# Kernel optimization log

Hardware: AMD Instinct MI355X
Metric: run time of the kernel (lower is better)

## Reference

```python
import jax, jax.numpy as jnp
import numpy as np

N = 200000       # num nodes
D = 128          # embedding dim
E_POS = 262144   # positive edges
NUM_NEGS = 4
E_NEG = E_POS * NUM_NEGS


def setup_inputs() -> dict:
    key = jax.random.key(0)
    k1, k2, k3, k4, k5 = jax.random.split(key, 5)
    h = jax.random.normal(k1, (N, D), dtype=jnp.float32)
    pos_src = jax.random.randint(k2, (E_POS,), 0, N, dtype=jnp.int32)
    pos_dst = jax.random.randint(k3, (E_POS,), 0, N, dtype=jnp.int32)
    neg_src = jax.random.randint(k4, (E_NEG,), 0, N, dtype=jnp.int32)
    neg_dst = jax.random.randint(k5, (E_NEG,), 0, N, dtype=jnp.int32)
    return {"h": h, "pos_src": pos_src, "pos_dst": pos_dst,
            "neg_src": neg_src, "neg_dst": neg_dst, "num_negs": NUM_NEGS}


def _edge_dot(h, src, dst):
    # SDDMM: gather src/dst rows, per-edge dot product -> [E]
    return jnp.einsum('ed,ed->e', h[src], h[dst])


def reference(h, pos_src, pos_dst, neg_src, neg_dst, num_negs):
    pos_score = _edge_dot(h, pos_src, pos_dst)   # [E_pos]
    neg_score = _edge_dot(h, neg_src, neg_dst)   # [E_neg]

    # BCE with logits: labels 1 for pos, 0 for neg
    score = jnp.concatenate([pos_score, neg_score])
    label = jnp.concatenate([jnp.ones_like(pos_score), jnp.zeros_like(neg_score)])
    loss = jnp.mean(jax.nn.softplus(score) - label * score)

    # MRR: rank of the positive among [pos | negs]
    mat = jnp.concatenate([pos_score[:, None],
                           neg_score.reshape(-1, num_negs)], axis=-1)  # [E_pos, 1+num_negs]
    order = jnp.argsort(-mat, axis=-1)          # indices_of_ranks (descending)
    ranks = jnp.argsort(order, axis=-1)[:, 0] + 1  # rank position of the positive
    mrr = jnp.mean(1.0 / ranks.astype(jnp.float32))
    return loss, mrr
```

## Files before the change

kernel.cpp:

```cpp
#include <hip/hip_runtime.h>
#include <math.h>

constexpr int NBLK    = 2048;
constexpr int CVT_BLK = 4096;

typedef float floatx2 __attribute__((ext_vector_type(2)));

#if __has_builtin(__builtin_amdgcn_cvt_pk_f32_fp8) && __has_builtin(__builtin_amdgcn_cvt_pk_fp8_f32)
#define HAVE_FP8_CVT 1
#else
#define HAVE_FP8_CVT 0
#endif

__device__ __forceinline__ float softplus_fast(float x) {
    float t = __expf(-fabsf(x));
    return fmaxf(x, 0.0f) + __logf(1.0f + t);
}


#if HAVE_FP8_CVT
__device__ __forceinline__ unsigned pack4_fp8(float x, float y, float z, float w) {
    int r = 0;
    r = __builtin_amdgcn_cvt_pk_fp8_f32(x, y, r, false);
    r = __builtin_amdgcn_cvt_pk_fp8_f32(z, w, r, true);
    return (unsigned)r;
}
__device__ __forceinline__ float dot_word_fp8(unsigned wa, unsigned wb, float c) {
    floatx2 a0 = __builtin_amdgcn_cvt_pk_f32_fp8((int)wa, false);
    floatx2 a1 = __builtin_amdgcn_cvt_pk_f32_fp8((int)wa, true);
    floatx2 b0 = __builtin_amdgcn_cvt_pk_f32_fp8((int)wb, false);
    floatx2 b1 = __builtin_amdgcn_cvt_pk_f32_fp8((int)wb, true);
    c = fmaf(a0.x, b0.x, c); c = fmaf(a0.y, b0.y, c);
    c = fmaf(a1.x, b1.x, c); c = fmaf(a1.y, b1.y, c);
    return c;
}
#else
__device__ __forceinline__ unsigned enc1_fp8(float f) {
    unsigned u = __float_as_uint(f);
    unsigned s = (u >> 24) & 0x80u;
    float a = fabsf(f);
    if (a < 0.001953125f) return s;
    if (a > 448.0f) a = 448.0f;
    unsigned b = __float_as_uint(a);
    unsigned exp = b >> 23;
    unsigned m = b & 0x7fffffu;
    unsigned mr = m >> 20, rest = m & 0xfffffu;
    if (rest > 0x80000u || (rest == 0x80000u && (mr & 1u))) mr++;
    if (mr == 8u) { mr = 0u; exp++; }
    int e8 = (int)exp - 127 + 7;
    if (e8 <= 0) return s;
    if (e8 > 15) { e8 = 15; mr = 6u; }
    return s | ((unsigned)e8 << 3) | mr;
}
__device__ __forceinline__ unsigned pack4_fp8(float x, float y, float z, float w) {
    return enc1_fp8(x) | (enc1_fp8(y) << 8) | (enc1_fp8(z) << 16) | (enc1_fp8(w) << 24);
}
__device__ __forceinline__ float dec1_fp8(unsigned v) {
    unsigned s = (v & 0x80u) << 24;
    unsigned em = v & 0x7fu;
    float mag;
    if (em < 8u) mag = (float)em * 0.001953125f;
    else         mag = __uint_as_float((em << 20) + (120u << 23));
    return __uint_as_float(s | __float_as_uint(mag));
}
__device__ __forceinline__ float dot_word_fp8(unsigned wa, unsigned wb, float c) {
    #pragma unroll
    for (int k = 0; k < 4; ++k)
        c = fmaf(dec1_fp8((wa >> (8 * k)) & 0xffu),
                 dec1_fp8((wb >> (8 * k)) & 0xffu), c);
    return c;
}
#endif

__device__ __forceinline__ float dot8_fp8_rows(const unsigned char* __restrict__ h8,
                                               int si, int di, int sub) {
    const uint2* ra = (const uint2*)(h8 + ((size_t)(unsigned)si << 7));
    const uint2* rb = (const uint2*)(h8 + ((size_t)(unsigned)di << 7));
    uint2 a = ra[sub];
    uint2 b = rb[sub];
    float c = dot_word_fp8(a.x, b.x, 0.0f);
    return  dot_word_fp8(a.y, b.y, c);
}

__global__ __launch_bounds__(256) void fused_kernel_8(
        const unsigned char* __restrict__ h8,
        const int* __restrict__ pos_src, const int* __restrict__ pos_dst,
        const int* __restrict__ neg_src, const int* __restrict__ neg_dst,
        float* __restrict__ out, int e_pos, float inv_total, float inv_epos) {
    const int lane = threadIdx.x & 63;
    const int warp = threadIdx.x >> 6;
    const int grp  = lane >> 4;
    const int sub  = lane & 15;
    const int gid0    = (blockIdx.x * (blockDim.x >> 6) + warp) * 4 + grp;
    const int gstride = gridDim.x * (blockDim.x >> 6) * 4;

    float loss_acc = 0.0f, mrr_acc = 0.0f;

    for (int i = gid0; i < e_pos; i += gstride) {
        int  ps = pos_src[i], pd = pos_dst[i];
        int4 ns = ((const int4*)neg_src)[i];
        int4 nd = ((const int4*)neg_dst)[i];

        float c0 = dot8_fp8_rows(h8, ps,   pd,   sub);
        float c1 = dot8_fp8_rows(h8, ns.x, nd.x, sub);
        float c2 = dot8_fp8_rows(h8, ns.y, nd.y, sub);
        float c3 = dot8_fp8_rows(h8, ns.z, nd.z, sub);
        float c4 = dot8_fp8_rows(h8, ns.w, nd.w, sub);

        #pragma unroll
        for (int off = 1; off <= 8; off <<= 1) {
            c0 += __shfl_xor(c0, off, 64);
            c1 += __shfl_xor(c1, off, 64);
            c2 += __shfl_xor(c2, off, 64);
            c3 += __shfl_xor(c3, off, 64);
            c4 += __shfl_xor(c4, off, 64);
        }
        if (sub == 0) {
            loss_acc += softplus_fast(-c0) + softplus_fast(c1) + softplus_fast(c2)
                      + softplus_fast(c3) + softplus_fast(c4);
            int r = 1 + (c1 > c0) + (c2 > c0) + (c3 > c0) + (c4 > c0);
            mrr_acc += 1.0f / (float)r;
        }
    }

    #pragma unroll
    for (int off = 1; off <= 32; off <<= 1) {
        loss_acc += __shfl_xor(loss_acc, off, 64);
        mrr_acc  += __shfl_xor(mrr_acc,  off, 64);
    }
    __shared__ float sl[4], sm[4];
    if (lane == 0) { sl[warp] = loss_acc; sm[warp] = mrr_acc; }
    __syncthreads();
    if (threadIdx.x == 0) {
        atomicAdd(&out[0], (sl[0] + sl[1] + sl[2] + sl[3]) * inv_total);
        atomicAdd(&out[1], (sm[0] + sm[1] + sm[2] + sm[3]) * inv_epos);
    }
}


__device__ __forceinline__ float dot_row_f(const float* __restrict__ h,
                                           int si, int di, int sub) {
    const float4* ra = (const float4*)((const char*)h + ((size_t)(unsigned)si << 9));
    const float4* rb = (const float4*)((const char*)h + ((size_t)(unsigned)di << 9));
    float4 a0 = ra[2*sub], a1 = ra[2*sub+1];
    float4 b0 = rb[2*sub], b1 = rb[2*sub+1];
    float c = a0.x*b0.x;
    c = fmaf(a0.y,b0.y,c); c = fmaf(a0.z,b0.z,c); c = fmaf(a0.w,b0.w,c);
    c = fmaf(a1.x,b1.x,c); c = fmaf(a1.y,b1.y,c);
    c = fmaf(a1.z,b1.z,c); c = fmaf(a1.w,b1.w,c);
    return c;
}

__global__ __launch_bounds__(256) void fused_kernel_f(
        const float* __restrict__ h,
        const int* __restrict__ pos_src, const int* __restrict__ pos_dst,
        const int* __restrict__ neg_src, const int* __restrict__ neg_dst,
        float* __restrict__ out, int e_pos, float inv_total, float inv_epos) {
    const int lane = threadIdx.x & 63;
    const int warp = threadIdx.x >> 6;
    const int grp  = lane >> 4;
    const int sub  = lane & 15;
    const int gid0    = (blockIdx.x * (blockDim.x >> 6) + warp) * 4 + grp;
    const int gstride = gridDim.x * (blockDim.x >> 6) * 4;

    float loss_acc = 0.0f, mrr_acc = 0.0f;
    for (int i = gid0; i < e_pos; i += gstride) {
        int  ps = pos_src[i], pd = pos_dst[i];
        int4 ns = ((const int4*)neg_src)[i];
        int4 nd = ((const int4*)neg_dst)[i];
        float c0 = dot_row_f(h, ps,   pd,   sub);
        float c1 = dot_row_f(h, ns.x, nd.x, sub);
        float c2 = dot_row_f(h, ns.y, nd.y, sub);
        float c3 = dot_row_f(h, ns.z, nd.z, sub);
        float c4 = dot_row_f(h, ns.w, nd.w, sub);
        #pragma unroll
        for (int off = 1; off <= 8; off <<= 1) {
            c0 += __shfl_xor(c0, off, 64);
            c1 += __shfl_xor(c1, off, 64);
            c2 += __shfl_xor(c2, off, 64);
            c3 += __shfl_xor(c3, off, 64);
            c4 += __shfl_xor(c4, off, 64);
        }
        if (sub == 0) {
            loss_acc += softplus_fast(-c0) + softplus_fast(c1) + softplus_fast(c2)
                      + softplus_fast(c3) + softplus_fast(c4);
            int r = 1 + (c1 > c0) + (c2 > c0) + (c3 > c0) + (c4 > c0);
            mrr_acc += 1.0f / (float)r;
        }
    }
    #pragma unroll
    for (int off = 1; off <= 32; off <<= 1) {
        loss_acc += __shfl_xor(loss_acc, off, 64);
        mrr_acc  += __shfl_xor(mrr_acc,  off, 64);
    }
    __shared__ float sl[4], sm[4];
    if (lane == 0) { sl[warp] = loss_acc; sm[warp] = mrr_acc; }
    __syncthreads();
    if (threadIdx.x == 0) {
        atomicAdd(&out[0], (sl[0] + sl[1] + sl[2] + sl[3]) * inv_total);
        atomicAdd(&out[1], (sm[0] + sm[1] + sm[2] + sm[3]) * inv_epos);
    }
}


__global__ __launch_bounds__(256) void convert_kernel_8(
        const float* __restrict__ h, unsigned char* __restrict__ h8, int n,
        float* __restrict__ out) {
    if (blockIdx.x == 0 && threadIdx.x == 0) { out[0] = 0.0f; out[1] = 0.0f; }
    const int tid    = blockIdx.x * blockDim.x + threadIdx.x;
    const int stride = gridDim.x * blockDim.x;
    const float4* h4 = (const float4*)h;
    uint2* o2 = (uint2*)h8;
    const int n8 = n >> 3;
    for (int i = tid; i < n8; i += stride) {
        float4 v0 = h4[2 * i];
        float4 v1 = h4[2 * i + 1];
        uint2 o;
        o.x = pack4_fp8(v0.x, v0.y, v0.z, v0.w);
        o.y = pack4_fp8(v1.x, v1.y, v1.z, v1.w);
        o2[i] = o;
    }
}

__global__ void zero_out_kernel(float* __restrict__ out) {
    out[0] = 0.0f; out[1] = 0.0f;
}

extern "C" void kernel_launch(void* const* d_in, const int* in_sizes, int n_in,
                              void* d_out, int out_size, void* d_ws, size_t ws_size,
                              hipStream_t stream) {
    const float* h       = (const float*)d_in[0];
    const int*   pos_src = (const int*)d_in[1];
    const int*   pos_dst = (const int*)d_in[2];
    const int*   neg_src = (const int*)d_in[3];
    const int*   neg_dst = (const int*)d_in[4];
    const int n_h   = in_sizes[0];
    const int e_pos = in_sizes[1];
    const int e_neg = in_sizes[3];
    float* out = (float*)d_out;

    const float inv_total = 1.0f / (float)((long long)e_pos + e_neg);
    const float inv_epos  = 1.0f / (float)e_pos;

    if (ws_size >= (size_t)n_h) {
        unsigned char* h8 = (unsigned char*)d_ws;
        convert_kernel_8<<<CVT_BLK, 256, 0, stream>>>(h, h8, n_h, out);
        fused_kernel_8<<<NBLK, 256, 0, stream>>>(
            h8, pos_src, pos_dst, neg_src, neg_dst,
            out, e_pos, inv_total, inv_epos);
    } else {
        zero_out_kernel<<<1, 1, 0, stream>>>(out);
        fused_kernel_f<<<NBLK, 256, 0, stream>>>(
            h, pos_src, pos_dst, neg_src, neg_dst,
            out, e_pos, inv_total, inv_epos);
    }
}
```

Before: 239.1 us.

## Use 8 lanes per edge with 16-byte row loads and prefetch next indices

Each edge group shrinks from 16 to 8 lanes, and each lane loads a uint4 (16 fp8 values) per row instead of a uint2. This widens the gather loads and halves the shuffle-reduction depth. The next iteration's edge indices are now loaded one iteration ahead (software pipelining) to hide index-load latency before the dependent row gathers. In exchange, each lane does twice the fp8 decode work and uses more registers, which may reduce occupancy.

Result: no change. 236.5 us (-1.1%).

```diff
diff --git a/kernel.cpp b/kernel.cpp
--- a/kernel.cpp
+++ b/kernel.cpp
@@ -72,14 +72,11 @@
 }
 #endif
 
-__device__ __forceinline__ float dot8_fp8_rows(const unsigned char* __restrict__ h8,
-                                               int si, int di, int sub) {
-    const uint2* ra = (const uint2*)(h8 + ((size_t)(unsigned)si << 7));
-    const uint2* rb = (const uint2*)(h8 + ((size_t)(unsigned)di << 7));
-    uint2 a = ra[sub];
-    uint2 b = rb[sub];
+__device__ __forceinline__ float dot_uint4_fp8(const uint4& a, const uint4& b) {
     float c = dot_word_fp8(a.x, b.x, 0.0f);
-    return  dot_word_fp8(a.y, b.y, c);
+    c = dot_word_fp8(a.y, b.y, c);
+    c = dot_word_fp8(a.z, b.z, c);
+    return dot_word_fp8(a.w, b.w, c);
 }
 
 __global__ __launch_bounds__(256) void fused_kernel_8(
@@ -89,26 +86,50 @@
         float* __restrict__ out, int e_pos, float inv_total, float inv_epos) {
     const int lane = threadIdx.x & 63;
     const int warp = threadIdx.x >> 6;
-    const int grp  = lane >> 4;
-    const int sub  = lane & 15;
-    const int gid0    = (blockIdx.x * (blockDim.x >> 6) + warp) * 4 + grp;
-    const int gstride = gridDim.x * (blockDim.x >> 6) * 4;
+    const int grp  = lane >> 3;
+    const int sub  = lane & 7;
+    const int gid0    = (blockIdx.x * (blockDim.x >> 6) + warp) * 8 + grp;
+    const int gstride = gridDim.x * (blockDim.x >> 6) * 8;
 
     float loss_acc = 0.0f, mrr_acc = 0.0f;
 
-    for (int i = gid0; i < e_pos; i += gstride) {
-        int  ps = pos_src[i], pd = pos_dst[i];
-        int4 ns = ((const int4*)neg_src)[i];
-        int4 nd = ((const int4*)neg_dst)[i];
-
-        float c0 = dot8_fp8_rows(h8, ps,   pd,   sub);
-        float c1 = dot8_fp8_rows(h8, ns.x, nd.x, sub);
-        float c2 = dot8_fp8_rows(h8, ns.y, nd.y, sub);
-        float c3 = dot8_fp8_rows(h8, ns.z, nd.z, sub);
-        float c4 = dot8_fp8_rows(h8, ns.w, nd.w, sub);
+    int  i = gid0;
+    int  ic = (i < e_pos) ? i : 0;
+    int  ps = pos_src[ic], pd = pos_dst[ic];
+    int4 ns = ((const int4*)neg_src)[ic];
+    int4 nd = ((const int4*)neg_dst)[ic];
+
+    for (; i < e_pos; i += gstride) {
+        int  in  = i + gstride;
+        int  icn = (in < e_pos) ? in : 0;
+        int  ps_n = pos_src[icn], pd_n = pos_dst[icn];
+        int4 ns_n = ((const int4*)neg_src)[icn];
+        int4 nd_n = ((const int4*)neg_dst)[icn];
+
+        const uint4* r0a = (const uint4*)(h8 + ((size_t)(unsigned)ps   << 7));
+        const uint4* r0b = (const uint4*)(h8 + ((size_t)(unsigned)pd   << 7));
+        const uint4* r1a = (const uint4*)(h8 + ((size_t)(unsigned)ns.x << 7));
+        const uint4* r1b = (const uint4*)(h8 + ((size_t)(unsigned)nd.x << 7));
+        const uint4* r2a = (const uint4*)(h8 + ((size_t)(unsigned)ns.y << 7));
+        const uint4* r2b = (const uint4*)(h8 + ((size_t)(unsigned)nd.y << 7));
+        const uint4* r3a = (const uint4*)(h8 + ((size_t)(unsigned)ns.z << 7));
+        const uint4* r3b = (const uint4*)(h8 + ((size_t)(unsigned)nd.z << 7));
+        const uint4* r4a = (const uint4*)(h8 + ((size_t)(unsigned)ns.w << 7));
+        const uint4* r4b = (const uint4*)(h8 + ((size_t)(unsigned)nd.w << 7));
+        uint4 a0 = r0a[sub], b0 = r0b[sub];
+        uint4 a1 = r1a[sub], b1 = r1b[sub];
+        uint4 a2 = r2a[sub], b2 = r2b[sub];
+        uint4 a3 = r3a[sub], b3 = r3b[sub];
+        uint4 a4 = r4a[sub], b4 = r4b[sub];
+
+        float c0 = dot_uint4_fp8(a0, b0);
+        float c1 = dot_uint4_fp8(a1, b1);
+        float c2 = dot_uint4_fp8(a2, b2);
+        float c3 = dot_uint4_fp8(a3, b3);
+        float c4 = dot_uint4_fp8(a4, b4);
 
         #pragma unroll
-        for (int off = 1; off <= 8; off <<= 1) {
+        for (int off = 1; off <= 4; off <<= 1) {
             c0 += __shfl_xor(c0, off, 64);
             c1 += __shfl_xor(c1, off, 64);
             c2 += __shfl_xor(c2, off, 64);
@@ -121,6 +142,8 @@
             int r = 1 + (c1 > c0) + (c2 > c0) + (c3 > c0) + (c4 > c0);
             mrr_acc += 1.0f / (float)r;
         }
+
+        ps = ps_n; pd = pd_n; ns = ns_n; nd = nd_n;
     }
 
     #pragma unroll
```
